# Kernel optimization log

Hardware: AMD Instinct MI355X
Metric: run time of the kernel (lower is better)

Reference implementation:

```python
import jax, jax.numpy as jnp
import numpy as np
import math

E = 1024      # embed_dim
H = 16        # num_heads
D = 32        # head_dim = E // H // 2
DEPTH = 12
LAMBDA_INIT = 0.8 - 0.6 * math.exp(-0.3 * DEPTH)
B, T = 4, 1024
EPS = 1e-5


def setup_inputs() -> dict:
    key = jax.random.key(0)
    ks = jax.random.split(key, 10)
    s = 0.02  # realistic init scale for weight matrices
    return {
        "x": jax.random.normal(ks[0], (B, T, E), jnp.float32),
        "Wq": jax.random.normal(ks[1], (E, E), jnp.float32) * s,
        "Wk": jax.random.normal(ks[2], (E, E), jnp.float32) * s,
        "Wv": jax.random.normal(ks[3], (E, E), jnp.float32) * s,
        "Wo": jax.random.normal(ks[4], (E, E), jnp.float32) * s,
        "lambda_q1": jax.random.normal(ks[5], (D,), jnp.float32) * 0.1,
        "lambda_k1": jax.random.normal(ks[6], (D,), jnp.float32) * 0.1,
        "lambda_q2": jax.random.normal(ks[7], (D,), jnp.float32) * 0.1,
        "lambda_k2": jax.random.normal(ks[8], (D,), jnp.float32) * 0.1,
        "g": jnp.ones((2 * D,), jnp.float32),  # subln affine weight
    }


def reference(x, Wq, Wk, Wv, Wo, lambda_q1, lambda_k1, lambda_q2, lambda_k2, g):
    b, t, _ = x.shape
    scaling = D ** -0.5
    # projections (torch Linear: x @ W.T), split into 2H half-width q/k heads
    q = (x @ Wq.T).reshape(b, t, 2 * H, D).transpose(0, 2, 1, 3) * scaling  # [b,2H,t,D]
    k = (x @ Wk.T).reshape(b, t, 2 * H, D).transpose(0, 2, 1, 3)            # [b,2H,t,D]
    v = (x @ Wv.T).reshape(b, t, H, 2 * D).transpose(0, 2, 1, 3)            # [b,H,t,2D]
    # dual score maps, fp32 softmax
    aw = jnp.einsum('bhqd,bhkd->bhqk', q, k)               # [b,2H,t,t]
    aw = jnp.nan_to_num(aw)
    aw = jax.nn.softmax(aw.astype(jnp.float32), axis=-1).astype(q.dtype)
    # scalar lambda
    lam1 = jnp.exp(jnp.sum(lambda_q1 * lambda_k1))
    lam2 = jnp.exp(jnp.sum(lambda_q2 * lambda_k2))
    lam = lam1 - lam2 + LAMBDA_INIT
    # differential subtract of the paired softmax maps
    aw = aw.reshape(b, H, 2, t, t)
    aw = aw[:, :, 0] - lam * aw[:, :, 1]                   # [b,H,t,t]
    attn = jnp.einsum('bhqk,bhkd->bhqd', aw, v)            # [b,H,t,2D]
    # per-head RMSNorm over 2D channel dim (affine)
    attn = attn * jax.lax.rsqrt(jnp.mean(attn * attn, axis=-1, keepdims=True) + EPS) * g
    attn = attn * (1.0 - LAMBDA_INIT)
    attn = attn.transpose(0, 2, 1, 3).reshape(b, t, H * 2 * D)  # [b,t,E]
    return attn @ Wo.T
```

## Files before the change

kernel.cpp:

```cpp
#include <hip/hip_runtime.h>
#include <math.h>

#define E_   1024
#define H_   16
#define B_   4
#define T_   1024
#define LAMBDA_INIT 0.783605766532f
#define SCALE_Q 0.17677669529663687f

typedef short s16x8 __attribute__((ext_vector_type(8)));
typedef float f32x4 __attribute__((ext_vector_type(4)));

__device__ inline ushort f2bf(float x) {
    unsigned u = __builtin_bit_cast(unsigned, x);
    u += 0x7fffu + ((u >> 16) & 1u);
    return (ushort)(u >> 16);
}

__device__ inline uint f2bf2(float lo, float hi) {
#if __has_builtin(__builtin_amdgcn_cvt_pk_bf16_f32)
    typedef __bf16 bf16x2_t __attribute__((ext_vector_type(2)));
    bf16x2_t r = __builtin_amdgcn_cvt_pk_bf16_f32(lo, hi);
    return __builtin_bit_cast(uint, r);
#else
    uint ul = __builtin_bit_cast(uint, lo);
    uint uh = __builtin_bit_cast(uint, hi);
    ul += 0x7fffu + ((ul >> 16) & 1u);
    uh += 0x7fffu + ((uh >> 16) & 1u);
    return __builtin_amdgcn_perm(uh, ul, 0x07060302u);
#endif
}

__device__ inline void gl_lds16(const ushort* g, ushort* l) {
    __builtin_amdgcn_global_load_lds((const __attribute__((address_space(1))) void*)g,
                                     (__attribute__((address_space(3))) void*)l,
                                     16, 0, 0);
}

__global__ __launch_bounds__(256) void cast_x(const float* __restrict__ in,
                                              ushort* __restrict__ out)
{
    int i = (blockIdx.x * 256 + threadIdx.x) * 8;
    float4 a = *(const float4*)&in[i];
    float4 b = *(const float4*)&in[i + 4];
    union { ushort u[8]; uint4 v; } o;
    o.u[0] = f2bf(a.x); o.u[1] = f2bf(a.y); o.u[2] = f2bf(a.z); o.u[3] = f2bf(a.w);
    o.u[4] = f2bf(b.x); o.u[5] = f2bf(b.y); o.u[6] = f2bf(b.z); o.u[7] = f2bf(b.w);
    *(uint4*)&out[i] = o.v;
}

__global__ __launch_bounds__(256) void cast_w4(
    const float* __restrict__ w0, const float* __restrict__ w1,
    const float* __restrict__ w2, const float* __restrict__ w3,
    ushort* __restrict__ o0, ushort* __restrict__ o1,
    ushort* __restrict__ o2, ushort* __restrict__ o3)
{
    const float* in = blockIdx.y == 0 ? w0 : (blockIdx.y == 1 ? w1 : (blockIdx.y == 2 ? w2 : w3));
    ushort* out = blockIdx.y == 0 ? o0 : (blockIdx.y == 1 ? o1 : (blockIdx.y == 2 ? o2 : o3));
    int i = (blockIdx.x * 256 + threadIdx.x) * 8;
    float4 a = *(const float4*)&in[i];
    float4 b = *(const float4*)&in[i + 4];
    union { ushort u[8]; uint4 v; } o;
    o.u[0] = f2bf(a.x); o.u[1] = f2bf(a.y); o.u[2] = f2bf(a.z); o.u[3] = f2bf(a.w);
    o.u[4] = f2bf(b.x); o.u[5] = f2bf(b.y); o.u[6] = f2bf(b.z); o.u[7] = f2bf(b.w);
    *(uint4*)&out[i] = o.v;
}

__global__ void lam_kernel(const float* __restrict__ lq1, const float* __restrict__ lk1,
                           const float* __restrict__ lq2, const float* __restrict__ lk2,
                           float* __restrict__ lamp)
{
    int l = threadIdx.x;
    float p1 = 0.f, p2 = 0.f;
    if (l < 32) { p1 = lq1[l] * lk1[l]; p2 = lq2[l] * lk2[l]; }
    #pragma unroll
    for (int off = 32; off; off >>= 1) {
        p1 += __shfl_xor(p1, off);
        p2 += __shfl_xor(p2, off);
    }
    if (l == 0) lamp[0] = expf(p1) - expf(p2) + LAMBDA_INIT;
}

__global__ __launch_bounds__(256) void gemm_qkv(
    const ushort* __restrict__ Xb, const ushort* __restrict__ Wqb,
    const ushort* __restrict__ Wkb, const ushort* __restrict__ Wvb,
    ushort* __restrict__ QKV)
{
    __shared__ ushort As[128 * 32];
    __shared__ ushort Ws[128 * 32];
    const int tid = threadIdx.x;
    const int wave = tid >> 6, lane = tid & 63;
    const int l15 = lane & 15, quad = lane >> 4;
    const int bm = blockIdx.y * 128;
    const int bng = blockIdx.x * 128;
    const int region = bng >> 10;
    const ushort* W = region == 0 ? Wqb : (region == 1 ? Wkb : Wvb);
    const float scale = region == 0 ? SCALE_Q : 1.0f;
    const int wn = bng & 1023;
    const int lrow = lane >> 2;
    const int lcol = (lane & 3) * 8;

    f32x4 acc[4][4] = {};
    const int wr = wave >> 1, wc = wave & 1;

    for (int k0 = 0; k0 < 1024; k0 += 32) {
        #pragma unroll
        for (int p = 0; p < 2; ++p) {
            int i = wave + 4 * p;
            gl_lds16(&Xb[(size_t)(bm + i * 16 + lrow) * 1024 + k0 + lcol], &As[i * 512]);
            gl_lds16(&W [(size_t)(wn + i * 16 + lrow) * 1024 + k0 + lcol], &Ws[i * 512]);
        }
        __syncthreads();
        s16x8 a[4], b[4];
        #pragma unroll
        for (int i = 0; i < 4; ++i)
            a[i] = *(const s16x8*)&As[(wr * 64 + i * 16 + l15) * 32 + quad * 8];
        #pragma unroll
        for (int j = 0; j < 4; ++j)
            b[j] = *(const s16x8*)&Ws[(wc * 64 + j * 16 + l15) * 32 + quad * 8];
        #pragma unroll
        for (int i = 0; i < 4; ++i)
            #pragma unroll
            for (int j = 0; j < 4; ++j)
                acc[i][j] = __builtin_amdgcn_mfma_f32_16x16x32_bf16(a[i], b[j], acc[i][j], 0, 0, 0);
        __syncthreads();
    }

    #pragma unroll
    for (int i = 0; i < 4; ++i)
        #pragma unroll
        for (int j = 0; j < 4; ++j)
            #pragma unroll
            for (int r = 0; r < 4; ++r) {
                int row = bm + wr * 64 + i * 16 + quad * 4 + r;
                int col = bng + wc * 64 + j * 16 + l15;
                QKV[(size_t)row * 3072 + col] = f2bf(acc[i][j][r] * scale);
            }
}

__global__ __launch_bounds__(256) void gemm_out(
    const ushort* __restrict__ Ab, const ushort* __restrict__ Wob,
    float* __restrict__ C)
{
    __shared__ ushort As[64 * 32];
    __shared__ ushort Ws[128 * 32];
    const int tid = threadIdx.x;
    const int wave = tid >> 6, lane = tid & 63;
    const int l15 = lane & 15, quad = lane >> 4;
    const int bm = blockIdx.y * 64;
    const int bn = blockIdx.x * 128;
    const int lrow = lane >> 2;
    const int lcol = (lane & 3) * 8;

    f32x4 acc[2][4] = {};
    const int wr = wave >> 1, wc = wave & 1;

    for (int k0 = 0; k0 < 1024; k0 += 32) {
        gl_lds16(&Ab[(size_t)(bm + wave * 16 + lrow) * 1024 + k0 + lcol], &As[wave * 512]);
        #pragma unroll
        for (int p = 0; p < 2; ++p) {
            int i = wave + 4 * p;
            gl_lds16(&Wob[(size_t)(bn + i * 16 + lrow) * 1024 + k0 + lcol], &Ws[i * 512]);
        }
        __syncthreads();
        s16x8 a[2], b[4];
        #pragma unroll
        for (int i = 0; i < 2; ++i)
            a[i] = *(const s16x8*)&As[(wr * 32 + i * 16 + l15) * 32 + quad * 8];
        #pragma unroll
        for (int j = 0; j < 4; ++j)
            b[j] = *(const s16x8*)&Ws[(wc * 64 + j * 16 + l15) * 32 + quad * 8];
        #pragma unroll
        for (int i = 0; i < 2; ++i)
            #pragma unroll
            for (int j = 0; j < 4; ++j)
                acc[i][j] = __builtin_amdgcn_mfma_f32_16x16x32_bf16(a[i], b[j], acc[i][j], 0, 0, 0);
        __syncthreads();
    }

    #pragma unroll
    for (int i = 0; i < 2; ++i)
        #pragma unroll
        for (int j = 0; j < 4; ++j)
            #pragma unroll
            for (int r = 0; r < 4; ++r) {
                int row = bm + wr * 32 + i * 16 + quad * 4 + r;
                int col = bn + wc * 64 + j * 16 + l15;
                C[(size_t)row * 1024 + col] = acc[i][j][r];
            }
}

__global__ __launch_bounds__(256) void transpose_v(
    const ushort* __restrict__ QKV, ushort* __restrict__ Vt)
{
    __shared__ ushort Ls[64][72];
    const int tid = threadIdx.x;
    const int m0 = blockIdx.x * 64;
    const int b  = m0 >> 10;
    const int t0 = m0 & 1023;
    const int e0 = blockIdx.y * 64;
    #pragma unroll
    for (int p = 0; p < 2; ++p) {
        int idx = tid + 256 * p;
        int r = idx >> 3, seg = (idx & 7) * 8;
        *(uint4*)&Ls[r][seg] =
            *(const uint4*)&QKV[(size_t)(m0 + r) * 3072 + 2048 + e0 + seg];
    }
    __syncthreads();
    #pragma unroll
    for (int p = 0; p < 2; ++p) {
        int idx = tid + 256 * p;
        int er = idx >> 3, ts = (idx & 7) * 8;
        union { ushort u[8]; uint4 v; } o;
        #pragma unroll
        for (int i = 0; i < 8; ++i) o.u[i] = Ls[ts + i][er];
        *(uint4*)&Vt[((size_t)b * E_ + e0 + er) * T_ + t0 + ts] = o.v;
    }
}

__global__ __launch_bounds__(256) void diff_attn(
    const ushort* __restrict__ QKV, const ushort* __restrict__ Vt,
    const float* __restrict__ g, const float* __restrict__ lamp,
    ushort* __restrict__ O)
{
    __shared__ __align__(16) ushort Ks[64][72];
    __shared__ __align__(16) ushort Vts[64][72];
    __shared__ __align__(16) ushort QP[9216];

    const int tid  = threadIdx.x;
    const int lane = tid & 63;
    const int wave = tid >> 6;
    const int l15  = lane & 15;
    const int quad = lane >> 4;

    const int blk = blockIdx.x;
    const int qt = blk & 7;
    const int h  = (blk >> 3) & 15;
    const int b  = blk >> 7;
    const int q0 = qt * 128;
    const int hoff = h * 64;
    const size_t rowbase = (size_t)b * T_;
    const size_t vtbase = ((size_t)b * E_ + hoff) * T_;

    const ushort* Qg = QKV;
    const ushort* Kg = QKV + 1024;

    #pragma unroll
    for (int p = 0; p < 4; ++p) {
        int idx = tid + 256 * p;
        int r = idx >> 3, seg = (idx & 7) * 8;
        *(uint4*)&QP[r * 72 + seg] =
            *(const uint4*)&Qg[(rowbase + q0 + r) * 3072 + hoff + seg];
    }
    const float lam = lamp[0];
    float4 gv[4];
    #pragma unroll
    for (int jt = 0; jt < 4; ++jt) gv[jt] = *(const float4*)&g[jt * 16 + quad * 4];
    __syncthreads();

    s16x8 aq[2][2];
    #pragma unroll
    for (int c = 0; c < 2; ++c)
        #pragma unroll
        for (int rt = 0; rt < 2; ++rt)
            aq[c][rt] = *(const s16x8*)&QP[(wave * 32 + rt * 16 + l15) * 72 + c * 32 + quad * 8];

    const f32x4 zf = {0.f, 0.f, 0.f, 0.f};
    f32x4 o[2][2][4];
    #pragma unroll
    for (int c = 0; c < 2; ++c)
        #pragma unroll
        for (int rt = 0; rt < 2; ++rt)
            #pragma unroll
            for (int jt = 0; jt < 4; ++jt) o[c][rt][jt] = zf;
    float lsum[2][2] = {};

    for (int kt = 0; kt < T_ / 64; ++kt) {
        __syncthreads();
        #pragma unroll
        for (int p = 0; p < 2; ++p) {
            int idx = tid + 256 * p;
            int r = idx >> 3, seg = (idx & 7) * 8;
            *(uint4*)&Ks[r][seg] =
                *(const uint4*)&Kg[(rowbase + kt * 64 + r) * 3072 + hoff + seg];
            *(uint4*)&Vts[r][seg] =
                *(const uint4*)&Vt[vtbase + (size_t)r * T_ + kt * 64 + seg];
        }
        __syncthreads();

        s16x8 va[4][2];
        #pragma unroll
        for (int jt = 0; jt < 4; ++jt)
            #pragma unroll
            for (int h2 = 0; h2 < 2; ++h2)
                va[jt][h2] = *(const s16x8*)&Vts[jt * 16 + l15][h2 * 32 + quad * 8];

        #pragma unroll
        for (int c = 0; c < 2; ++c) {
            s16x8 ka[4];
            #pragma unroll
            for (int jk = 0; jk < 4; ++jk)
                ka[jk] = *(const s16x8*)&Ks[jk * 16 + l15][c * 32 + quad * 8];

            #pragma unroll
            for (int rt = 0; rt < 2; ++rt) {
                ushort* Pt = &QP[(wave * 2 + rt) * 1152];
                f32x4 S[4];
                #pragma unroll
                for (int jk = 0; jk < 4; ++jk)
                    S[jk] = __builtin_amdgcn_mfma_f32_16x16x32_bf16(ka[jk], aq[c][rt], zf, 0, 0, 0);
                float part = 0.f;
                #pragma unroll
                for (int jk = 0; jk < 4; ++jk) {
                    float e0 = __expf(S[jk][0]);
                    float e1 = __expf(S[jk][1]);
                    float e2 = __expf(S[jk][2]);
                    float e3 = __expf(S[jk][3]);
                    part += (e0 + e1) + (e2 + e3);
                    uint2 pk;
                    pk.x = f2bf2(e0, e1);
                    pk.y = f2bf2(e2, e3);
                    *(uint2*)&Pt[l15 * 72 + jk * 16 + quad * 4] = pk;
                }
                lsum[c][rt] += part;
                #pragma unroll
                for (int h2 = 0; h2 < 2; ++h2) {
                    s16x8 pf = *(const s16x8*)&Pt[l15 * 72 + h2 * 32 + quad * 8];
                    #pragma unroll
                    for (int jt = 0; jt < 4; ++jt)
                        o[c][rt][jt] = __builtin_amdgcn_mfma_f32_16x16x32_bf16(
                            va[jt][h2], pf, o[c][rt][jt], 0, 0, 0);
                }
            }
        }
    }

    #pragma unroll
    for (int c = 0; c < 2; ++c)
        #pragma unroll
        for (int rt = 0; rt < 2; ++rt) {
            float s = lsum[c][rt];
            s += __shfl_xor(s, 16);
            s += __shfl_xor(s, 32);
            lsum[c][rt] = s;
        }

    const float fin = 1.f - LAMBDA_INIT;
    #pragma unroll
    for (int rt = 0; rt < 2; ++rt) {
        float i0 = 1.f / lsum[0][rt];
        float i1 = lam / lsum[1][rt];
        float val[4][4];
        float ssq = 0.f;
        #pragma unroll
        for (int jt = 0; jt < 4; ++jt)
            #pragma unroll
            for (int r = 0; r < 4; ++r) {
                float v = o[0][rt][jt][r] * i0 - o[1][rt][jt][r] * i1;
                val[jt][r] = v;
                ssq += v * v;
            }
        ssq += __shfl_xor(ssq, 16);
        ssq += __shfl_xor(ssq, 32);
        float sc = rsqrtf(ssq * (1.f / 64.f) + 1e-5f) * fin;
        size_t rowoff = (rowbase + q0 + wave * 32 + rt * 16 + l15) * 1024 + hoff;
        #pragma unroll
        for (int jt = 0; jt < 4; ++jt) {
            float gx = gv[jt].x, gy = gv[jt].y, gz = gv[jt].z, gw = gv[jt].w;
            uint p01 = f2bf2(val[jt][0] * sc * gx, val[jt][1] * sc * gy);
            uint p23 = f2bf2(val[jt][2] * sc * gz, val[jt][3] * sc * gw);
            *(uint*)&O[rowoff + jt * 16 + quad * 4 + 0] = p01;
            *(uint*)&O[rowoff + jt * 16 + quad * 4 + 2] = p23;
        }
    }
}

extern "C" void kernel_launch(void* const* d_in, const int* in_sizes, int n_in,
                              void* d_out, int out_size, void* d_ws, size_t ws_size,
                              hipStream_t stream)
{
    const float* x   = (const float*)d_in[0];
    const float* Wq  = (const float*)d_in[1];
    const float* Wk  = (const float*)d_in[2];
    const float* Wv  = (const float*)d_in[3];
    const float* Wo  = (const float*)d_in[4];
    const float* lq1 = (const float*)d_in[5];
    const float* lk1 = (const float*)d_in[6];
    const float* lq2 = (const float*)d_in[7];
    const float* lk2 = (const float*)d_in[8];
    const float* g   = (const float*)d_in[9];
    float* out = (float*)d_out;

    const int M = B_ * T_;
    const size_t ME = (size_t)M * E_;
    const size_t EE = (size_t)E_ * E_;
    ushort* xb  = (ushort*)d_ws;
    ushort* Wqb = xb  + ME;
    ushort* Wkb = Wqb + EE;
    ushort* Wvb = Wkb + EE;
    ushort* Wob = Wvb + EE;
    ushort* QKV = Wob + EE;
    ushort* Vtb = QKV + (size_t)M * 3072;
    ushort* Ab  = Vtb + ME;
    float*  lamp = (float*)(Ab + ME);

    cast_x<<<ME / (256 * 8), 256, 0, stream>>>(x, xb);
    cast_w4<<<dim3(EE / (256 * 8), 4), 256, 0, stream>>>(Wq, Wk, Wv, Wo, Wqb, Wkb, Wvb, Wob);
    lam_kernel<<<1, 64, 0, stream>>>(lq1, lk1, lq2, lk2, lamp);
    gemm_qkv<<<dim3(24, 32), 256, 0, stream>>>(xb, Wqb, Wkb, Wvb, QKV);
    transpose_v<<<dim3(M / 64, E_ / 64), 256, 0, stream>>>(QKV, Vtb);
    diff_attn<<<B_ * H_ * (T_ / 128), 256, 0, stream>>>(QKV, Vtb, g, lamp, Ab);
    gemm_out<<<dim3(8, 64), 256, 0, stream>>>(Ab, Wob, out);
}
```

Baseline: 223.1 us.

## Merge prep kernels and retile diff_attn with register-prefetched K/V tiles

```diff
diff --git a/kernel.cpp b/kernel.cpp
--- a/kernel.cpp
+++ b/kernel.cpp
@@ -7,6 +7,7 @@
 #define T_   1024
 #define LAMBDA_INIT 0.783605766532f
 #define SCALE_Q 0.17677669529663687f
+#define SK 68
 
 typedef short s16x8 __attribute__((ext_vector_type(8)));
 typedef float f32x4 __attribute__((ext_vector_type(4)));
@@ -37,48 +38,47 @@
                                      16, 0, 0);
 }
 
-__global__ __launch_bounds__(256) void cast_x(const float* __restrict__ in,
-                                              ushort* __restrict__ out)
-{
-    int i = (blockIdx.x * 256 + threadIdx.x) * 8;
+__global__ __launch_bounds__(256) void prep(
+    const float* __restrict__ x,  const float* __restrict__ Wq,
+    const float* __restrict__ Wk, const float* __restrict__ Wv,
+    const float* __restrict__ Wo,
+    const float* __restrict__ lq1, const float* __restrict__ lk1,
+    const float* __restrict__ lq2, const float* __restrict__ lk2,
+    ushort* __restrict__ xb, ushort* __restrict__ Wqb, ushort* __restrict__ Wkb,
+    ushort* __restrict__ Wvb, ushort* __restrict__ Wob, float* __restrict__ lamp)
+{
+    const int blk = blockIdx.x;
+    const int tid = threadIdx.x;
+    if (blk >= 4096) {
+        if (tid < 64) {
+            float p1 = 0.f, p2 = 0.f;
+            if (tid < 32) { p1 = lq1[tid] * lk1[tid]; p2 = lq2[tid] * lk2[tid]; }
+            #pragma unroll
+            for (int off = 32; off; off >>= 1) {
+                p1 += __shfl_xor(p1, off);
+                p2 += __shfl_xor(p2, off);
+            }
+            if (tid == 0) lamp[0] = expf(p1) - expf(p2) + LAMBDA_INIT;
+        }
+        return;
+    }
+    const float* in;
+    ushort* out;
+    int base;
+    if (blk < 2048) { in = x; out = xb; base = blk; }
+    else {
+        int t = blk - 2048, w = t >> 9;
+        base = t & 511;
+        in  = w == 0 ? Wq  : (w == 1 ? Wk  : (w == 2 ? Wv  : Wo));
+        out = w == 0 ? Wqb : (w == 1 ? Wkb : (w == 2 ? Wvb : Wob));
+    }
+    int i = (base * 256 + tid) * 8;
     float4 a = *(const float4*)&in[i];
     float4 b = *(const float4*)&in[i + 4];
     union { ushort u[8]; uint4 v; } o;
     o.u[0] = f2bf(a.x); o.u[1] = f2bf(a.y); o.u[2] = f2bf(a.z); o.u[3] = f2bf(a.w);
     o.u[4] = f2bf(b.x); o.u[5] = f2bf(b.y); o.u[6] = f2bf(b.z); o.u[7] = f2bf(b.w);
     *(uint4*)&out[i] = o.v;
-}
-
-__global__ __launch_bounds__(256) void cast_w4(
-    const float* __restrict__ w0, const float* __restrict__ w1,
-    const float* __restrict__ w2, const float* __restrict__ w3,
-    ushort* __restrict__ o0, ushort* __restrict__ o1,
-    ushort* __restrict__ o2, ushort* __restrict__ o3)
-{
-    const float* in = blockIdx.y == 0 ? w0 : (blockIdx.y == 1 ? w1 : (blockIdx.y == 2 ? w2 : w3));
-    ushort* out = blockIdx.y == 0 ? o0 : (blockIdx.y == 1 ? o1 : (blockIdx.y == 2 ? o2 : o3));
-    int i = (blockIdx.x * 256 + threadIdx.x) * 8;
-    float4 a = *(const float4*)&in[i];
-    float4 b = *(const float4*)&in[i + 4];
-    union { ushort u[8]; uint4 v; } o;
-    o.u[0] = f2bf(a.x); o.u[1] = f2bf(a.y); o.u[2] = f2bf(a.z); o.u[3] = f2bf(a.w);
-    o.u[4] = f2bf(b.x); o.u[5] = f2bf(b.y); o.u[6] = f2bf(b.z); o.u[7] = f2bf(b.w);
-    *(uint4*)&out[i] = o.v;
-}
-
-__global__ void lam_kernel(const float* __restrict__ lq1, const float* __restrict__ lk1,
-                           const float* __restrict__ lq2, const float* __restrict__ lk2,
-                           float* __restrict__ lamp)
-{
-    int l = threadIdx.x;
-    float p1 = 0.f, p2 = 0.f;
-    if (l < 32) { p1 = lq1[l] * lk1[l]; p2 = lq2[l] * lk2[l]; }
-    #pragma unroll
-    for (int off = 32; off; off >>= 1) {
-        p1 += __shfl_xor(p1, off);
-        p2 += __shfl_xor(p2, off);
-    }
-    if (l == 0) lamp[0] = expf(p1) - expf(p2) + LAMBDA_INIT;
 }
 
 __global__ __launch_bounds__(256) void gemm_qkv(
@@ -218,14 +218,14 @@
     }
 }
 
-__global__ __launch_bounds__(256) void diff_attn(
+__global__ __launch_bounds__(256, 4) void diff_attn(
     const ushort* __restrict__ QKV, const ushort* __restrict__ Vt,
     const float* __restrict__ g, const float* __restrict__ lamp,
     ushort* __restrict__ O)
 {
-    __shared__ __align__(16) ushort Ks[64][72];
-    __shared__ __align__(16) ushort Vts[64][72];
-    __shared__ __align__(16) ushort QP[9216];
+    __shared__ __align__(16) ushort Ks[64 * SK];
+    __shared__ __align__(16) ushort Vts[64 * SK];
+    __shared__ __align__(16) ushort PtQ[4 * 2 * 16 * SK];
 
     const int tid  = threadIdx.x;
     const int lane = tid & 63;
@@ -234,10 +234,10 @@
     const int quad = lane >> 4;
 
     const int blk = blockIdx.x;
-    const int qt = blk & 7;
-    const int h  = (blk >> 3) & 15;
-    const int b  = blk >> 7;
-    const int q0 = qt * 128;
+    const int qt = blk & 15;
+    const int h  = (blk >> 4) & 15;
+    const int b  = blk >> 8;
+    const int q0 = qt * 64;
     const int hoff = h * 64;
     const size_t rowbase = (size_t)b * T_;
     const size_t vtbase = ((size_t)b * E_ + hoff) * T_;
@@ -245,12 +245,12 @@
     const ushort* Qg = QKV;
     const ushort* Kg = QKV + 1024;
 
-    #pragma unroll
-    for (int p = 0; p < 4; ++p) {
-        int idx = tid + 256 * p;
-        int r = idx >> 3, seg = (idx & 7) * 8;
-        *(uint4*)&QP[r * 72 + seg] =
+    {
+        int r = tid >> 2, seg = (tid & 3) * 16;
+        *(uint4*)&PtQ[r * SK + seg] =
             *(const uint4*)&Qg[(rowbase + q0 + r) * 3072 + hoff + seg];
+        *(uint4*)&PtQ[r * SK + seg + 8] =
+            *(const uint4*)&Qg[(rowbase + q0 + r) * 3072 + hoff + seg + 8];
     }
     const float lam = lamp[0];
     float4 gv[4];
@@ -258,120 +258,118 @@
     for (int jt = 0; jt < 4; ++jt) gv[jt] = *(const float4*)&g[jt * 16 + quad * 4];
     __syncthreads();
 
-    s16x8 aq[2][2];
+    s16x8 aq[2];
     #pragma unroll
     for (int c = 0; c < 2; ++c)
-        #pragma unroll
-        for (int rt = 0; rt < 2; ++rt)
-            aq[c][rt] = *(const s16x8*)&QP[(wave * 32 + rt * 16 + l15) * 72 + c * 32 + quad * 8];
+        aq[c] = *(const s16x8*)&PtQ[(wave * 16 + l15) * SK + c * 32 + quad * 8];
+    __syncthreads();
+
+    ushort* Pt0 = &PtQ[(wave * 2 + 0) * 16 * SK];
+    ushort* Pt1 = &PtQ[(wave * 2 + 1) * 16 * SK];
 
     const f32x4 zf = {0.f, 0.f, 0.f, 0.f};
-    f32x4 o[2][2][4];
-    #pragma unroll
-    for (int c = 0; c < 2; ++c)
-        #pragma unroll
-        for (int rt = 0; rt < 2; ++rt)
-            #pragma unroll
-            for (int jt = 0; jt < 4; ++jt) o[c][rt][jt] = zf;
-    float lsum[2][2] = {};
+    f32x4 o0[4] = {zf, zf, zf, zf};
+    f32x4 o1[4] = {zf, zf, zf, zf};
+    float lsum[2] = {0.f, 0.f};
+
+    const int r0 = tid >> 2, s0 = (tid & 3) * 16;
+    uint4 kr0, kr1, vr0, vr1;
+    {
+        size_t ko = (rowbase + 0 + r0) * 3072 + hoff + s0;
+        kr0 = *(const uint4*)&Kg[ko];
+        kr1 = *(const uint4*)&Kg[ko + 8];
+        size_t vo = vtbase + (size_t)r0 * T_ + 0 + s0;
+        vr0 = *(const uint4*)&Vt[vo];
+        vr1 = *(const uint4*)&Vt[vo + 8];
+    }
 
     for (int kt = 0; kt < T_ / 64; ++kt) {
         __syncthreads();
-        #pragma unroll
-        for (int p = 0; p < 2; ++p) {
-            int idx = tid + 256 * p;
-            int r = idx >> 3, seg = (idx & 7) * 8;
-            *(uint4*)&Ks[r][seg] =
-                *(const uint4*)&Kg[(rowbase + kt * 64 + r) * 3072 + hoff + seg];
-            *(uint4*)&Vts[r][seg] =
-                *(const uint4*)&Vt[vtbase + (size_t)r * T_ + kt * 64 + seg];
-        }
-        __syncthreads();
-
-        s16x8 va[4][2];
-        #pragma unroll
-        for (int jt = 0; jt < 4; ++jt)
-            #pragma unroll
-            for (int h2 = 0; h2 < 2; ++h2)
-                va[jt][h2] = *(const s16x8*)&Vts[jt * 16 + l15][h2 * 32 + quad * 8];
-
-        #pragma unroll
-        for (int c = 0; c < 2; ++c) {
-            s16x8 ka[4];
-            #pragma unroll
-            for (int jk = 0; jk < 4; ++jk)
-                ka[jk] = *(const s16x8*)&Ks[jk * 16 + l15][c * 32 + quad * 8];
-
-            #pragma unroll
-            for (int rt = 0; rt < 2; ++rt) {
-                ushort* Pt = &QP[(wave * 2 + rt) * 1152];
-                f32x4 S[4];
-                #pragma unroll
-                for (int jk = 0; jk < 4; ++jk)
-                    S[jk] = __builtin_amdgcn_mfma_f32_16x16x32_bf16(ka[jk], aq[c][rt], zf, 0, 0, 0);
-                float part = 0.f;
-                #pragma unroll
-                for (int jk = 0; jk < 4; ++jk) {
-                    float e0 = __expf(S[jk][0]);
-                    float e1 = __expf(S[jk][1]);
-                    float e2 = __expf(S[jk][2]);
-                    float e3 = __expf(S[jk][3]);
-                    part += (e0 + e1) + (e2 + e3);
-                    uint2 pk;
-                    pk.x = f2bf2(e0, e1);
-                    pk.y = f2bf2(e2, e3);
-                    *(uint2*)&Pt[l15 * 72 + jk * 16 + quad * 4] = pk;
-                }
-                lsum[c][rt] += part;
-                #pragma unroll
-                for (int h2 = 0; h2 < 2; ++h2) {
-                    s16x8 pf = *(const s16x8*)&Pt[l15 * 72 + h2 * 32 + quad * 8];
-                    #pragma unroll
-                    for (int jt = 0; jt < 4; ++jt)
-                        o[c][rt][jt] = __builtin_amdgcn_mfma_f32_16x16x32_bf16(
-                            va[jt][h2], pf, o[c][rt][jt], 0, 0, 0);
-                }
+        *(uint4*)&Ks[r0 * SK + s0]      = kr0;
+        *(uint4*)&Ks[r0 * SK + s0 + 8]  = kr1;
+        *(uint4*)&Vts[r0 * SK + s0]     = vr0;
+        *(uint4*)&Vts[r0 * SK + s0 + 8] = vr1;
+        __syncthreads();
+
+        {
+            int ktn = (kt + 1) & 15;
+            size_t ko = (rowbase + ktn * 64 + r0) * 3072 + hoff + s0;
+            kr0 = *(const uint4*)&Kg[ko];
+            kr1 = *(const uint4*)&Kg[ko + 8];
+            size_t vo = vtbase + (size_t)r0 * T_ + ktn * 64 + s0;
+            vr0 = *(const uint4*)&Vt[vo];
+            vr1 = *(const uint4*)&Vt[vo + 8];
+        }
+
+        f32x4 S0[4], S1[4];
+        #pragma unroll
+        for (int jk = 0; jk < 4; ++jk) {
+            s16x8 ka0 = *(const s16x8*)&Ks[(jk * 16 + l15) * SK + quad * 8];
+            s16x8 ka1 = *(const s16x8*)&Ks[(jk * 16 + l15) * SK + 32 + quad * 8];
+            S0[jk] = __builtin_amdgcn_mfma_f32_16x16x32_bf16(ka0, aq[0], zf, 0, 0, 0);
+            S1[jk] = __builtin_amdgcn_mfma_f32_16x16x32_bf16(ka1, aq[1], zf, 0, 0, 0);
+        }
+        float part0 = 0.f, part1 = 0.f;
+        #pragma unroll
+        for (int jk = 0; jk < 4; ++jk) {
+            float a0 = __expf(S0[jk][0]), a1 = __expf(S0[jk][1]);
+            float a2 = __expf(S0[jk][2]), a3 = __expf(S0[jk][3]);
+            float b0 = __expf(S1[jk][0]), b1 = __expf(S1[jk][1]);
+            float b2 = __expf(S1[jk][2]), b3 = __expf(S1[jk][3]);
+            part0 += (a0 + a1) + (a2 + a3);
+            part1 += (b0 + b1) + (b2 + b3);
+            uint2 pk0, pk1;
+            pk0.x = f2bf2(a0, a1); pk0.y = f2bf2(a2, a3);
+            pk1.x = f2bf2(b0, b1); pk1.y = f2bf2(b2, b3);
+            *(uint2*)&Pt0[l15 * SK + jk * 16 + quad * 4] = pk0;
+            *(uint2*)&Pt1[l15 * SK + jk * 16 + quad * 4] = pk1;
+        }
+        lsum[0] += part0;
+        lsum[1] += part1;
+        #pragma unroll
+        for (int h2 = 0; h2 < 2; ++h2) {
+            s16x8 pf0 = *(const s16x8*)&Pt0[l15 * SK + h2 * 32 + quad * 8];
+            s16x8 pf1 = *(const s16x8*)&Pt1[l15 * SK + h2 * 32 + quad * 8];
+            #pragma unroll
+            for (int jt = 0; jt < 4; ++jt) {
+                s16x8 va = *(const s16x8*)&Vts[(jt * 16 + l15) * SK + h2 * 32 + quad * 8];
+                o0[jt] = __builtin_amdgcn_mfma_f32_16x16x32_bf16(va, pf0, o0[jt], 0, 0, 0);
+                o1[jt] = __builtin_amdgcn_mfma_f32_16x16x32_bf16(va, pf1, o1[jt], 0, 0, 0);
             }
         }
     }
 
     #pragma unroll
-    for (int c = 0; c < 2; ++c)
-        #pragma unroll
-        for (int rt = 0; rt < 2; ++rt) {
-            float s = lsum[c][rt];
-            s += __shfl_xor(s, 16);
-            s += __shfl_xor(s, 32);
-            lsum[c][rt] = s;
-        }
+    for (int c = 0; c < 2; ++c) {
+        float s = lsum[c];
+        s += __shfl_xor(s, 16);
+        s += __shfl_xor(s, 32);
+        lsum[c] = s;
+    }
 
     const float fin = 1.f - LAMBDA_INIT;
-    #pragma unroll
-    for (int rt = 0; rt < 2; ++rt) {
-        float i0 = 1.f / lsum[0][rt];
-        float i1 = lam / lsum[1][rt];
-        float val[4][4];
-        float ssq = 0.f;
-        #pragma unroll
-        for (int jt = 0; jt < 4; ++jt)
-            #pragma unroll
-            for (int r = 0; r < 4; ++r) {
-                float v = o[0][rt][jt][r] * i0 - o[1][rt][jt][r] * i1;
-                val[jt][r] = v;
-                ssq += v * v;
-            }
-        ssq += __shfl_xor(ssq, 16);
-        ssq += __shfl_xor(ssq, 32);
-        float sc = rsqrtf(ssq * (1.f / 64.f) + 1e-5f) * fin;
-        size_t rowoff = (rowbase + q0 + wave * 32 + rt * 16 + l15) * 1024 + hoff;
-        #pragma unroll
-        for (int jt = 0; jt < 4; ++jt) {
-            float gx = gv[jt].x, gy = gv[jt].y, gz = gv[jt].z, gw = gv[jt].w;
-            uint p01 = f2bf2(val[jt][0] * sc * gx, val[jt][1] * sc * gy);
-            uint p23 = f2bf2(val[jt][2] * sc * gz, val[jt][3] * sc * gw);
-            *(uint*)&O[rowoff + jt * 16 + quad * 4 + 0] = p01;
-            *(uint*)&O[rowoff + jt * 16 + quad * 4 + 2] = p23;
-        }
+    float i0 = 1.f / lsum[0];
+    float i1 = lam / lsum[1];
+    float val[4][4];
+    float ssq = 0.f;
+    #pragma unroll
+    for (int jt = 0; jt < 4; ++jt)
+        #pragma unroll
+        for (int r = 0; r < 4; ++r) {
+            float v = o0[jt][r] * i0 - o1[jt][r] * i1;
+            val[jt][r] = v;
+            ssq += v * v;
+        }
+    ssq += __shfl_xor(ssq, 16);
+    ssq += __shfl_xor(ssq, 32);
+    float sc = rsqrtf(ssq * (1.f / 64.f) + 1e-5f) * fin;
+    size_t rowoff = (rowbase + q0 + wave * 16 + l15) * 1024 + hoff;
+    #pragma unroll
+    for (int jt = 0; jt < 4; ++jt) {
+        uint p01 = f2bf2(val[jt][0] * sc * gv[jt].x, val[jt][1] * sc * gv[jt].y);
+        uint p23 = f2bf2(val[jt][2] * sc * gv[jt].z, val[jt][3] * sc * gv[jt].w);
+        *(uint*)&O[rowoff + jt * 16 + quad * 4 + 0] = p01;
+        *(uint*)&O[rowoff + jt * 16 + quad * 4 + 2] = p23;
     }
 }
 
@@ -404,11 +402,10 @@
     ushort* Ab  = Vtb + ME;
     float*  lamp = (float*)(Ab + ME);
 
-    cast_x<<<ME / (256 * 8), 256, 0, stream>>>(x, xb);
-    cast_w4<<<dim3(EE / (256 * 8), 4), 256, 0, stream>>>(Wq, Wk, Wv, Wo, Wqb, Wkb, Wvb, Wob);
-    lam_kernel<<<1, 64, 0, stream>>>(lq1, lk1, lq2, lk2, lamp);
+    prep<<<4097, 256, 0, stream>>>(x, Wq, Wk, Wv, Wo, lq1, lk1, lq2, lk2,
+                                   xb, Wqb, Wkb, Wvb, Wob, lamp);
     gemm_qkv<<<dim3(24, 32), 256, 0, stream>>>(xb, Wqb, Wkb, Wvb, QKV);
     transpose_v<<<dim3(M / 64, E_ / 64), 256, 0, stream>>>(QKV, Vtb);
-    diff_attn<<<B_ * H_ * (T_ / 128), 256, 0, stream>>>(QKV, Vtb, g, lamp, Ab);
+    diff_attn<<<B_ * H_ * (T_ / 64), 256, 0, stream>>>(QKV, Vtb, g, lamp, Ab);
     gemm_out<<<dim3(8, 64), 256, 0, stream>>>(Ab, Wob, out);
 }
```

After: 214.2 us. 3.9% less time.
